# Kernel tuning notes

Measured on AMD Instinct MI355X. Metric: run time of the kernel, lower is better.

## Reference

```python
import jax, jax.numpy as jnp
import numpy as np

HIDDEN = 96


def setup_inputs() -> dict:
    key = jax.random.key(0)
    ks = jax.random.split(key, 7)
    B, T, H = 32, 16384, HIDDEN
    s = 1.0 / np.sqrt(H)  # torch LSTM init scale
    return {
        "x": jax.random.normal(ks[0], (B, T, 1), dtype=jnp.float32),
        "w_ih": jax.random.uniform(ks[1], (4 * H, 1), jnp.float32, -s, s),
        "w_hh": jax.random.uniform(ks[2], (4 * H, H), jnp.float32, -s, s),
        "b_ih": jax.random.uniform(ks[3], (4 * H,), jnp.float32, -s, s),
        "b_hh": jax.random.uniform(ks[4], (4 * H,), jnp.float32, -s, s),
        "w_dense": jax.random.uniform(ks[5], (1, H), jnp.float32, -s, s),
        "b_dense": jax.random.uniform(ks[6], (1,), jnp.float32, -s, s),
    }


def reference(x, w_ih, w_hh, b_ih, b_hh, w_dense, b_dense):
    # x: [B, T, 1]; single-layer LSTM (PyTorch gate order i, f, g, o),
    # zero initial hidden/cell state, then Linear(H -> 1) head.
    B, T, _ = x.shape
    H = w_hh.shape[1]
    b = b_ih + b_hh  # [4H]
    # Precompute input projection for all timesteps (input_size = 1).
    x_proj = jnp.einsum('btd,gd->btg', x, w_ih) + b  # [B, T, 4H]

    def step(carry, xp_t):
        h, c = carry
        gates = xp_t + h @ w_hh.T  # [B, 4H]
        i, f, g, o = jnp.split(gates, 4, axis=-1)
        i = jax.nn.sigmoid(i)
        f = jax.nn.sigmoid(f)
        g = jnp.tanh(g)
        o = jax.nn.sigmoid(o)
        c = f * c + i * g
        h = o * jnp.tanh(c)
        return (h, c), h

    h0 = jnp.zeros((B, H), dtype=x.dtype)
    c0 = jnp.zeros((B, H), dtype=x.dtype)
    _, hs = jax.lax.scan(step, (h0, c0), jnp.swapaxes(x_proj, 0, 1))  # hs: [T, B, H]
    hs = jnp.swapaxes(hs, 0, 1)  # [B, T, H]
    out = hs @ w_dense.T + b_dense  # [B, T, 1]; normalize_out=False -> no tanh
    return out
```

## Files before the change

### kernel.cpp

```cpp
#include <hip/hip_runtime.h>

typedef _Float16 h2 __attribute__((ext_vector_type(2)));

__device__ __forceinline__ h2 mkh2(float a, float b) {
    h2 r; r.x = (_Float16)a; r.y = (_Float16)b; return r;
}
__device__ __forceinline__ h2 bc(unsigned u) {
    union { unsigned u; h2 h; } c; c.u = u; return c.h;
}

template <int CTRL>
__device__ __forceinline__ float dpp_q(float v) {
    int i = __builtin_bit_cast(int, v);
    int r = __builtin_amdgcn_update_dpp(0, i, CTRL, 0xF, 0xF, true);
    return __builtin_bit_cast(float, r);
}

#define BARRIER() asm volatile("s_waitcnt lgkmcnt(0)\n\ts_barrier" ::: "memory")

#define DOT8(Q, i) do {                                               \
    aA0 = __builtin_amdgcn_fdot2(WA[4*i+0], bc(Q.x), aA0, false);     \
    aA1 = __builtin_amdgcn_fdot2(WA[4*i+1], bc(Q.y), aA1, false);     \
    aA2 = __builtin_amdgcn_fdot2(WA[4*i+2], bc(Q.z), aA2, false);     \
    aA3 = __builtin_amdgcn_fdot2(WA[4*i+3], bc(Q.w), aA3, false);     \
    aB0 = __builtin_amdgcn_fdot2(WB[4*i+0], bc(Q.x), aB0, false);     \
    aB1 = __builtin_amdgcn_fdot2(WB[4*i+1], bc(Q.y), aB1, false);     \
    aB2 = __builtin_amdgcn_fdot2(WB[4*i+2], bc(Q.z), aB2, false);     \
    aB3 = __builtin_amdgcn_fdot2(WB[4*i+3], bc(Q.w), aB3, false);     \
} while (0)

__device__ __forceinline__ float head_dot(const float* hrow, const float* wdp) {
    const float4* hr = reinterpret_cast<const float4*>(hrow);
    const float4* wv = reinterpret_cast<const float4*>(wdp);
    float a0 = 0.f, a1 = 0.f, a2 = 0.f, a3 = 0.f;
    #pragma unroll
    for (int k = 0; k < 24; k += 4) {
        float4 ha = hr[k], hb = hr[k + 1], hc = hr[k + 2], hd = hr[k + 3];
        float4 wa = wv[k], wb = wv[k + 1], wc = wv[k + 2], wd = wv[k + 3];
        a0 = fmaf(ha.w, wa.w, fmaf(ha.z, wa.z, fmaf(ha.y, wa.y, fmaf(ha.x, wa.x, a0))));
        a1 = fmaf(hb.w, wb.w, fmaf(hb.z, wb.z, fmaf(hb.y, wb.y, fmaf(hb.x, wb.x, a1))));
        a2 = fmaf(hc.w, wc.w, fmaf(hc.z, wc.z, fmaf(hc.y, wc.y, fmaf(hc.x, wc.x, a2))));
        a3 = fmaf(hd.w, wd.w, fmaf(hd.z, wd.z, fmaf(hd.y, wd.y, fmaf(hd.x, wd.x, a3))));
    }
    return (a0 + a1) + (a2 + a3);
}

__global__ __launch_bounds__(256)
void lstm_fused(
    const float* __restrict__ x,
    const float* __restrict__ w_ih,
    const float* __restrict__ w_hh,
    const float* __restrict__ b_ih,
    const float* __restrict__ b_hh,
    const float* __restrict__ w_dense,
    const float* __restrict__ b_dense,
    float* __restrict__ out,
    int T)
{
    const int tid  = threadIdx.x;
    const int lane = tid & 63;
    const int wv   = tid >> 6;

    __shared__ __align__(16) _Float16 hbuf[2][96];
    __shared__ __align__(16) float hist[2][64][100];

    if (tid < 96) { hbuf[0][tid] = (_Float16)0.f; hbuf[1][tid] = (_Float16)0.f; }

    const float* xrow = x + (size_t)blockIdx.x * T;
    float*       orow = out + (size_t)blockIdx.x * T;

    __syncthreads();

    if (wv < 3) {
        const int p = lane & 1;
        const int u = (wv << 5) | (lane >> 1);
        const int rowA = 96 * p + u;
        const int rowB = 96 * (2 + p) + u;

        h2 WA[48], WB[48];
        {
            const float4* ra = reinterpret_cast<const float4*>(w_hh + (size_t)rowA * 96);
            const float4* rb = reinterpret_cast<const float4*>(w_hh + (size_t)rowB * 96);
            #pragma unroll
            for (int q = 0; q < 24; ++q) {
                float4 fa = ra[q];
                WA[2*q]   = mkh2(fa.x, fa.y);
                WA[2*q+1] = mkh2(fa.z, fa.w);
            }
            #pragma unroll
            for (int q = 0; q < 24; ++q) {
                float4 fb = rb[q];
                WB[2*q]   = mkh2(fb.x, fb.y);
                WB[2*q+1] = mkh2(fb.z, fb.w);
            }
        }

        const float wihA  = w_ih[rowA];
        const float wihB  = w_ih[rowB];
        const float biasA = b_ih[rowA] + b_hh[rowA];
        const float biasB = b_ih[rowB] + b_hh[rowB];
        const float nkB = (p == 0) ? -2.885390082f : -1.442695041f;
        const float m1B = (p == 0) ? 2.f : 1.f;
        const float d1B = (p == 0) ? -1.f : 0.f;

        float c  = 0.f;
        float xs = xrow[0];

        #pragma unroll 1
        for (int t = 0; t < T; ++t) {
            int tn = (t + 1 < T) ? t + 1 : T - 1;
            float xs_n = xrow[tn];

            const uint4* hp = reinterpret_cast<const uint4*>(hbuf[(t & 1) ^ 1]);
            float aA0 = 0.f, aA1 = 0.f, aA2 = 0.f, aA3 = 0.f;
            float aB0 = 0.f, aB1 = 0.f, aB2 = 0.f, aB3 = 0.f;
            uint4 qA = hp[0], qB = hp[1], qC = hp[2];
            DOT8(qA, 0);  qA = hp[3];
            DOT8(qB, 1);  qB = hp[4];
            DOT8(qC, 2);  qC = hp[5];
            DOT8(qA, 3);  qA = hp[6];
            DOT8(qB, 4);  qB = hp[7];
            DOT8(qC, 5);  qC = hp[8];
            DOT8(qA, 6);  qA = hp[9];
            DOT8(qB, 7);  qB = hp[10];
            DOT8(qC, 8);  qC = hp[11];
            DOT8(qA, 9);
            DOT8(qB, 10);
            DOT8(qC, 11);

            float vA = (aA0 + aA1) + (aA2 + aA3);
            float vB = (aB0 + aB1) + (aB2 + aB3);
            float preA = vA + fmaf(xs, wihA, biasA);
            float preB = vB + fmaf(xs, wihB, biasB);
            float actA = __builtin_amdgcn_rcpf(1.f + __builtin_exp2f(preA * -1.442695041f));
            float actB = fmaf(m1B, __builtin_amdgcn_rcpf(1.f + __builtin_exp2f(preB * nkB)), d1B);

            float oA = dpp_q<0xB1>(actA);
            float oB = dpp_q<0xB1>(actB);

            if (p == 0) {
                c = fmaf(oA, c, actA * actB);
                float th = fmaf(2.f, __builtin_amdgcn_rcpf(1.f + __builtin_exp2f(c * -2.885390082f)), -1.f);
                float h  = oB * th;
                hbuf[t & 1][u] = (_Float16)h;
                hist[(t >> 6) & 1][t & 63][u] = h;
            }
            BARRIER();
            xs = xs_n;
        }
    } else {
        const float bd = b_dense[0];
        #pragma unroll 1
        for (int t = 0; t < T; ++t) {
            if (t && (t & 63) == 0) {
                const int buf = ((t >> 6) - 1) & 1;
                float a = head_dot(&hist[buf][lane][0], w_dense);
                orow[t - 64 + lane] = a + bd;
            }
            BARRIER();
        }
        const int T0 = ((T - 1) >> 6) << 6;
        if (lane < T - T0) {
            const int buf = (T0 >> 6) & 1;
            float a = head_dot(&hist[buf][lane][0], w_dense);
            orow[T0 + lane] = a + bd;
        }
    }
}

extern "C" void kernel_launch(void* const* d_in, const int* in_sizes, int n_in,
                              void* d_out, int out_size, void* d_ws, size_t ws_size,
                              hipStream_t stream) {
    const float* x   = (const float*)d_in[0];
    const float* wih = (const float*)d_in[1];
    const float* whh = (const float*)d_in[2];
    const float* bih = (const float*)d_in[3];
    const float* bhh = (const float*)d_in[4];
    const float* wd  = (const float*)d_in[5];
    const float* bd  = (const float*)d_in[6];
    float* out = (float*)d_out;

    const int B = 32;
    const int T = in_sizes[0] / B;

    lstm_fused<<<dim3(B), dim3(256), 0, stream>>>(x, wih, whh, bih, bhh, wd, bd, out, T);
}
```

Measured before the change: 7.999 ms.

## Compute recurrent matvec with MFMA 16x16x32 f16 across six gate waves

Moves the per-step h·W_hh product from per-lane fdot2 chains onto MFMA instructions. The work is spread over six compute waves of 16 hidden units each, with the activation scale constants folded into the weights and bias. Gate values are picked out of the MFMA accumulator lanes and exchanged between lanes with DPP. The block grows to 448 threads, which adds waves to every per-step barrier. The MFMA approach wastes most of the matrix width, because only one batch column per block is useful.

```diff
diff --git a/kernel.cpp b/kernel.cpp
--- a/kernel.cpp
+++ b/kernel.cpp
@@ -1,13 +1,7 @@
 #include <hip/hip_runtime.h>
 
-typedef _Float16 h2 __attribute__((ext_vector_type(2)));
-
-__device__ __forceinline__ h2 mkh2(float a, float b) {
-    h2 r; r.x = (_Float16)a; r.y = (_Float16)b; return r;
-}
-__device__ __forceinline__ h2 bc(unsigned u) {
-    union { unsigned u; h2 h; } c; c.u = u; return c.h;
-}
+typedef _Float16 f16x8 __attribute__((ext_vector_type(8)));
+typedef float    f32x4 __attribute__((ext_vector_type(4)));
 
 template <int CTRL>
 __device__ __forceinline__ float dpp_q(float v) {
@@ -17,17 +11,6 @@
 }
 
 #define BARRIER() asm volatile("s_waitcnt lgkmcnt(0)\n\ts_barrier" ::: "memory")
-
-#define DOT8(Q, i) do {                                               \
-    aA0 = __builtin_amdgcn_fdot2(WA[4*i+0], bc(Q.x), aA0, false);     \
-    aA1 = __builtin_amdgcn_fdot2(WA[4*i+1], bc(Q.y), aA1, false);     \
-    aA2 = __builtin_amdgcn_fdot2(WA[4*i+2], bc(Q.z), aA2, false);     \
-    aA3 = __builtin_amdgcn_fdot2(WA[4*i+3], bc(Q.w), aA3, false);     \
-    aB0 = __builtin_amdgcn_fdot2(WB[4*i+0], bc(Q.x), aB0, false);     \
-    aB1 = __builtin_amdgcn_fdot2(WB[4*i+1], bc(Q.y), aB1, false);     \
-    aB2 = __builtin_amdgcn_fdot2(WB[4*i+2], bc(Q.z), aB2, false);     \
-    aB3 = __builtin_amdgcn_fdot2(WB[4*i+3], bc(Q.w), aB3, false);     \
-} while (0)
 
 __device__ __forceinline__ float head_dot(const float* hrow, const float* wdp) {
     const float4* hr = reinterpret_cast<const float4*>(hrow);
@@ -45,7 +28,7 @@
     return (a0 + a1) + (a2 + a3);
 }
 
-__global__ __launch_bounds__(256)
+__global__ __launch_bounds__(448)
 void lstm_fused(
     const float* __restrict__ x,
     const float* __restrict__ w_ih,
@@ -71,37 +54,41 @@
 
     __syncthreads();
 
-    if (wv < 3) {
-        const int p = lane & 1;
-        const int u = (wv << 5) | (lane >> 1);
-        const int rowA = 96 * p + u;
-        const int rowB = 96 * (2 + p) + u;
+    if (wv < 6) {
+        const int g    = lane & 3;
+        const int uq   = lane >> 2;
+        const int u    = wv * 16 + uq;
+        const int arow = lane & 15;
+        const int kg   = lane >> 4;
 
-        h2 WA[48], WB[48];
-        {
-            const float4* ra = reinterpret_cast<const float4*>(w_hh + (size_t)rowA * 96);
-            const float4* rb = reinterpret_cast<const float4*>(w_hh + (size_t)rowB * 96);
+        f16x8 A_[4][3];
+        #pragma unroll
+        for (int ct = 0; ct < 4; ++ct) {
+            const float nk = (ct == 2) ? -2.885390082f : -1.442695041f;
+            const float* rp = w_hh + (size_t)(96 * ct + 16 * wv + arow) * 96 + kg * 8;
             #pragma unroll
-            for (int q = 0; q < 24; ++q) {
-                float4 fa = ra[q];
-                WA[2*q]   = mkh2(fa.x, fa.y);
-                WA[2*q+1] = mkh2(fa.z, fa.w);
-            }
+            for (int kt = 0; kt < 3; ++kt)
+                #pragma unroll
+                for (int i = 0; i < 8; ++i)
+                    A_[ct][kt][i] = (_Float16)(nk * rp[kt * 32 + i]);
+        }
+
+        float wihs[4][4], biass[4][4];
+        #pragma unroll
+        for (int ct = 0; ct < 4; ++ct) {
+            const float nk = (ct == 2) ? -2.885390082f : -1.442695041f;
             #pragma unroll
-            for (int q = 0; q < 24; ++q) {
-                float4 fb = rb[q];
-                WB[2*q]   = mkh2(fb.x, fb.y);
-                WB[2*q+1] = mkh2(fb.z, fb.w);
+            for (int q = 0; q < 4; ++q) {
+                int j = 96 * ct + 16 * wv + kg * 4 + q;
+                wihs[ct][q]  = nk * w_ih[j];
+                biass[ct][q] = nk * (b_ih[j] + b_hh[j]);
             }
         }
 
-        const float wihA  = w_ih[rowA];
-        const float wihB  = w_ih[rowB];
-        const float biasA = b_ih[rowA] + b_hh[rowA];
-        const float biasB = b_ih[rowB] + b_hh[rowB];
-        const float nkB = (p == 0) ? -2.885390082f : -1.442695041f;
-        const float m1B = (p == 0) ? 2.f : 1.f;
-        const float d1B = (p == 0) ? -1.f : 0.f;
+        const float m1 = (g == 2) ? 2.f : 1.f;
+        const float d1 = (g == 2) ? -1.f : 0.f;
+        const bool  g1 = (g & 1) != 0, g2 = (g & 2) != 0;
+        const bool  u1 = (uq & 1) != 0, u2 = (uq & 2) != 0;
 
         float c  = 0.f;
         float xs = xrow[0];
@@ -111,37 +98,49 @@
             int tn = (t + 1 < T) ? t + 1 : T - 1;
             float xs_n = xrow[tn];
 
-            const uint4* hp = reinterpret_cast<const uint4*>(hbuf[(t & 1) ^ 1]);
-            float aA0 = 0.f, aA1 = 0.f, aA2 = 0.f, aA3 = 0.f;
-            float aB0 = 0.f, aB1 = 0.f, aB2 = 0.f, aB3 = 0.f;
-            uint4 qA = hp[0], qB = hp[1], qC = hp[2];
-            DOT8(qA, 0);  qA = hp[3];
-            DOT8(qB, 1);  qB = hp[4];
-            DOT8(qC, 2);  qC = hp[5];
-            DOT8(qA, 3);  qA = hp[6];
-            DOT8(qB, 4);  qB = hp[7];
-            DOT8(qC, 5);  qC = hp[8];
-            DOT8(qA, 6);  qA = hp[9];
-            DOT8(qB, 7);  qB = hp[10];
-            DOT8(qC, 8);  qC = hp[11];
-            DOT8(qA, 9);
-            DOT8(qB, 10);
-            DOT8(qC, 11);
+            f32x4 D0, D1, D2, D3;
+            #pragma unroll
+            for (int q = 0; q < 4; ++q) {
+                D0[q] = fmaf(xs, wihs[0][q], biass[0][q]);
+                D1[q] = fmaf(xs, wihs[1][q], biass[1][q]);
+                D2[q] = fmaf(xs, wihs[2][q], biass[2][q]);
+                D3[q] = fmaf(xs, wihs[3][q], biass[3][q]);
+            }
 
-            float vA = (aA0 + aA1) + (aA2 + aA3);
-            float vB = (aB0 + aB1) + (aB2 + aB3);
-            float preA = vA + fmaf(xs, wihA, biasA);
-            float preB = vB + fmaf(xs, wihB, biasB);
-            float actA = __builtin_amdgcn_rcpf(1.f + __builtin_exp2f(preA * -1.442695041f));
-            float actB = fmaf(m1B, __builtin_amdgcn_rcpf(1.f + __builtin_exp2f(preB * nkB)), d1B);
+            const _Float16* hb = hbuf[(t & 1) ^ 1];
+            f16x8 B0 = *(const f16x8*)&hb[ 0 + kg * 8];
+            f16x8 B1 = *(const f16x8*)&hb[32 + kg * 8];
+            f16x8 B2 = *(const f16x8*)&hb[64 + kg * 8];
 
-            float oA = dpp_q<0xB1>(actA);
-            float oB = dpp_q<0xB1>(actB);
+            D0 = __builtin_amdgcn_mfma_f32_16x16x32_f16(A_[0][0], B0, D0, 0, 0, 0);
+            D1 = __builtin_amdgcn_mfma_f32_16x16x32_f16(A_[1][0], B0, D1, 0, 0, 0);
+            D2 = __builtin_amdgcn_mfma_f32_16x16x32_f16(A_[2][0], B0, D2, 0, 0, 0);
+            D3 = __builtin_amdgcn_mfma_f32_16x16x32_f16(A_[3][0], B0, D3, 0, 0, 0);
+            D0 = __builtin_amdgcn_mfma_f32_16x16x32_f16(A_[0][1], B1, D0, 0, 0, 0);
+            D1 = __builtin_amdgcn_mfma_f32_16x16x32_f16(A_[1][1], B1, D1, 0, 0, 0);
+            D2 = __builtin_amdgcn_mfma_f32_16x16x32_f16(A_[2][1], B1, D2, 0, 0, 0);
+            D3 = __builtin_amdgcn_mfma_f32_16x16x32_f16(A_[3][1], B1, D3, 0, 0, 0);
+            D0 = __builtin_amdgcn_mfma_f32_16x16x32_f16(A_[0][2], B2, D0, 0, 0, 0);
+            D1 = __builtin_amdgcn_mfma_f32_16x16x32_f16(A_[1][2], B2, D1, 0, 0, 0);
+            D2 = __builtin_amdgcn_mfma_f32_16x16x32_f16(A_[2][2], B2, D2, 0, 0, 0);
+            D3 = __builtin_amdgcn_mfma_f32_16x16x32_f16(A_[3][2], B2, D3, 0, 0, 0);
 
-            if (p == 0) {
-                c = fmaf(oA, c, actA * actB);
+            float s0 = g1 ? (g2 ? D3[0] : D1[0]) : (g2 ? D2[0] : D0[0]);
+            float s1 = g1 ? (g2 ? D3[1] : D1[1]) : (g2 ? D2[1] : D0[1]);
+            float s2 = g1 ? (g2 ? D3[2] : D1[2]) : (g2 ? D2[2] : D0[2]);
+            float s3 = g1 ? (g2 ? D3[3] : D1[3]) : (g2 ? D2[3] : D0[3]);
+            float pre = u1 ? (u2 ? s3 : s1) : (u2 ? s2 : s0);
+
+            float actv = fmaf(m1, __builtin_amdgcn_rcpf(1.f + __builtin_exp2f(pre)), d1);
+
+            float x1 = dpp_q<0xB1>(actv);
+            float x2 = dpp_q<0x4E>(actv);
+            float x3 = dpp_q<0x1B>(actv);
+
+            if (g == 0) {
+                c = fmaf(x1, c, actv * x2);
                 float th = fmaf(2.f, __builtin_amdgcn_rcpf(1.f + __builtin_exp2f(c * -2.885390082f)), -1.f);
-                float h  = oB * th;
+                float h  = x3 * th;
                 hbuf[t & 1][u] = (_Float16)h;
                 hist[(t >> 6) & 1][t & 63][u] = h;
             }
@@ -183,5 +182,5 @@
     const int B = 32;
     const int T = in_sizes[0] / B;
 
-    lstm_fused<<<dim3(B), dim3(256), 0, stream>>>(x, wih, whh, bih, bhh, wd, bd, out, T);
+    lstm_fused<<<dim3(B), dim3(448), 0, stream>>>(x, wih, whh, bih, bhh, wd, bd, out, T);
 }
```

Measured after the change: 8.378 ms. +4.7%, slower.

## Replace per-step block barrier with LDS flag spin-wait synchronization

Applied to the files above, without the earlier changes.

Swaps the per-timestep s_barrier across all four waves for sequence counters in shared memory. Each recurrent wave publishes its step and spins until the other two have caught up, and the head wave waits only at 64-step window boundaries. The goal is to take the head wave out of every step's barrier and let waves run with looser coupling. The cost is extra LDS polling traffic each step, and the spin loops have iteration caps that could silently break correctness if they time out. Visibility of the LDS writes relies only on lgkmcnt waits and volatile accesses.

```diff
diff --git a/kernel.cpp b/kernel.cpp
--- a/kernel.cpp
+++ b/kernel.cpp
@@ -15,8 +15,6 @@
     int r = __builtin_amdgcn_update_dpp(0, i, CTRL, 0xF, 0xF, true);
     return __builtin_bit_cast(float, r);
 }
-
-#define BARRIER() asm volatile("s_waitcnt lgkmcnt(0)\n\ts_barrier" ::: "memory")
 
 #define DOT8(Q, i) do {                                               \
     aA0 = __builtin_amdgcn_fdot2(WA[4*i+0], bc(Q.x), aA0, false);     \
@@ -28,6 +26,8 @@
     aB2 = __builtin_amdgcn_fdot2(WB[4*i+2], bc(Q.z), aB2, false);     \
     aB3 = __builtin_amdgcn_fdot2(WB[4*i+3], bc(Q.w), aB3, false);     \
 } while (0)
+
+#define LGKM0() asm volatile("s_waitcnt lgkmcnt(0)" ::: "memory")
 
 __device__ __forceinline__ float head_dot(const float* hrow, const float* wdp) {
     const float4* hr = reinterpret_cast<const float4*>(hrow);
@@ -63,13 +63,17 @@
 
     __shared__ __align__(16) _Float16 hbuf[2][96];
     __shared__ __align__(16) float hist[2][64][100];
+    __shared__ __align__(16) unsigned seqf[4];
 
     if (tid < 96) { hbuf[0][tid] = (_Float16)0.f; hbuf[1][tid] = (_Float16)0.f; }
+    if (tid < 4)  seqf[tid] = 0u;
 
     const float* xrow = x + (size_t)blockIdx.x * T;
     float*       orow = out + (size_t)blockIdx.x * T;
 
     __syncthreads();
+
+    volatile unsigned* sf = seqf;
 
     if (wv < 3) {
         const int p = lane & 1;
@@ -108,6 +112,24 @@
 
         #pragma unroll 1
         for (int t = 0; t < T; ++t) {
+            {
+                const unsigned need = (unsigned)t;
+                #pragma unroll 1
+                for (int spin = 0; spin < (1 << 18); ++spin) {
+                    if (sf[0] >= need && sf[1] >= need && sf[2] >= need) break;
+                }
+            }
+            if ((t & 63) == 0) {
+                const int w = t >> 6;
+                if (w >= 2) {
+                    const unsigned need = (unsigned)(w - 1);
+                    #pragma unroll 1
+                    for (int spin = 0; spin < (1 << 18); ++spin) {
+                        if (sf[3] >= need) break;
+                    }
+                }
+            }
+
             int tn = (t + 1 < T) ? t + 1 : T - 1;
             float xs_n = xrow[tn];
 
@@ -145,25 +167,37 @@
                 hbuf[t & 1][u] = (_Float16)h;
                 hist[(t >> 6) & 1][t & 63][u] = h;
             }
-            BARRIER();
+
+            LGKM0();
+            if (lane == 0) sf[wv] = (unsigned)(t + 1);
             xs = xs_n;
         }
     } else {
         const float bd = b_dense[0];
+        const int nwin = T >> 6;
         #pragma unroll 1
-        for (int t = 0; t < T; ++t) {
-            if (t && (t & 63) == 0) {
-                const int buf = ((t >> 6) - 1) & 1;
-                float a = head_dot(&hist[buf][lane][0], w_dense);
-                orow[t - 64 + lane] = a + bd;
-            }
-            BARRIER();
-        }
-        const int T0 = ((T - 1) >> 6) << 6;
-        if (lane < T - T0) {
-            const int buf = (T0 >> 6) & 1;
-            float a = head_dot(&hist[buf][lane][0], w_dense);
-            orow[T0 + lane] = a + bd;
+        for (int w = 0; w < nwin; ++w) {
+            const unsigned need = (unsigned)((w + 1) << 6);
+            #pragma unroll 1
+            for (int spin = 0; spin < (1 << 20); ++spin) {
+                if (sf[0] >= need && sf[1] >= need && sf[2] >= need) break;
+            }
+            float a = head_dot(&hist[w & 1][lane][0], w_dense);
+            orow[(w << 6) + lane] = a + bd;
+            LGKM0();
+            if (lane == 0) sf[3] = (unsigned)(w + 1);
+        }
+        const int T0 = nwin << 6;
+        if (T0 < T) {
+            const unsigned need = (unsigned)T;
+            #pragma unroll 1
+            for (int spin = 0; spin < (1 << 20); ++spin) {
+                if (sf[0] >= need && sf[1] >= need && sf[2] >= need) break;
+            }
+            if (lane < T - T0) {
+                float a = head_dot(&hist[nwin & 1][lane][0], w_dense);
+                orow[T0 + lane] = a + bd;
+            }
         }
     }
 }
```

Result: slower. 11.95 ms (+49.4%).

## Prefetch own-wave hidden-state chunks before the barrier to shorten the post-barrier LDS reads

Applied to the files above, without the earlier changes.

Each recurrent wave now issues LDS loads for the four h chunks it just wrote before hitting the per-step barrier. The barrier waits only until at most four LDS ops are outstanding, so those loads are in flight across it. After the barrier, only the other waves' eight chunks still need to be read. The W_hh register layout is rotated per wave so these prefetched chunks line up with the first dot products. The head wave keeps a full-drain barrier, and launch bounds now declare one block per CU. Correctness relies on in-order LDS counter semantics, so the earlier stores complete before the wave reaches the barrier.

```diff
diff --git a/kernel.cpp b/kernel.cpp
--- a/kernel.cpp
+++ b/kernel.cpp
@@ -16,8 +16,6 @@
     return __builtin_bit_cast(float, r);
 }
 
-#define BARRIER() asm volatile("s_waitcnt lgkmcnt(0)\n\ts_barrier" ::: "memory")
-
 #define DOT8(Q, i) do {                                               \
     aA0 = __builtin_amdgcn_fdot2(WA[4*i+0], bc(Q.x), aA0, false);     \
     aA1 = __builtin_amdgcn_fdot2(WA[4*i+1], bc(Q.y), aA1, false);     \
@@ -28,6 +26,9 @@
     aB2 = __builtin_amdgcn_fdot2(WB[4*i+2], bc(Q.z), aB2, false);     \
     aB3 = __builtin_amdgcn_fdot2(WB[4*i+3], bc(Q.w), aB3, false);     \
 } while (0)
+
+#define BARRIER4() asm volatile("s_waitcnt lgkmcnt(4)\n\ts_barrier" ::: "memory")
+#define BARRIER0() asm volatile("s_waitcnt lgkmcnt(0)\n\ts_barrier" ::: "memory")
 
 __device__ __forceinline__ float head_dot(const float* hrow, const float* wdp) {
     const float4* hr = reinterpret_cast<const float4*>(hrow);
@@ -45,7 +46,7 @@
     return (a0 + a1) + (a2 + a3);
 }
 
-__global__ __launch_bounds__(256)
+__global__ __launch_bounds__(256, 1)
 void lstm_fused(
     const float* __restrict__ x,
     const float* __restrict__ w_ih,
@@ -82,16 +83,14 @@
             const float4* ra = reinterpret_cast<const float4*>(w_hh + (size_t)rowA * 96);
             const float4* rb = reinterpret_cast<const float4*>(w_hh + (size_t)rowB * 96);
             #pragma unroll
-            for (int q = 0; q < 24; ++q) {
-                float4 fa = ra[q];
-                WA[2*q]   = mkh2(fa.x, fa.y);
-                WA[2*q+1] = mkh2(fa.z, fa.w);
-            }
-            #pragma unroll
-            for (int q = 0; q < 24; ++q) {
-                float4 fb = rb[q];
-                WB[2*q]   = mkh2(fb.x, fb.y);
-                WB[2*q+1] = mkh2(fb.z, fb.w);
+            for (int j = 0; j < 12; ++j) {
+                int cc = 4 * wv + j; if (cc >= 12) cc -= 12;
+                float4 fa = ra[2 * cc], ga = ra[2 * cc + 1];
+                WA[4*j+0] = mkh2(fa.x, fa.y); WA[4*j+1] = mkh2(fa.z, fa.w);
+                WA[4*j+2] = mkh2(ga.x, ga.y); WA[4*j+3] = mkh2(ga.z, ga.w);
+                float4 fb = rb[2 * cc], gb = rb[2 * cc + 1];
+                WB[4*j+0] = mkh2(fb.x, fb.y); WB[4*j+1] = mkh2(fb.z, fb.w);
+                WB[4*j+2] = mkh2(gb.x, gb.y); WB[4*j+3] = mkh2(gb.z, gb.w);
             }
         }
 
@@ -103,8 +102,21 @@
         const float m1B = (p == 0) ? 2.f : 1.f;
         const float d1B = (p == 0) ? -1.f : 0.f;
 
+        int c4  = 4*wv + 4;  if (c4  >= 12) c4  -= 12;
+        int c5  = 4*wv + 5;  if (c5  >= 12) c5  -= 12;
+        int c6  = 4*wv + 6;  if (c6  >= 12) c6  -= 12;
+        int c7  = 4*wv + 7;  if (c7  >= 12) c7  -= 12;
+        int c8  = 4*wv + 8;  if (c8  >= 12) c8  -= 12;
+        int c9  = 4*wv + 9;  if (c9  >= 12) c9  -= 12;
+        int c10 = 4*wv + 10; if (c10 >= 12) c10 -= 12;
+        int c11 = 4*wv + 11; if (c11 >= 12) c11 -= 12;
+
         float c  = 0.f;
         float xs = xrow[0];
+
+        const uint4* hp0 = reinterpret_cast<const uint4*>(hbuf[1]);
+        uint4 qO0 = hp0[4*wv + 0], qO1 = hp0[4*wv + 1];
+        uint4 qO2 = hp0[4*wv + 2], qO3 = hp0[4*wv + 3];
 
         #pragma unroll 1
         for (int t = 0; t < T; ++t) {
@@ -112,21 +124,14 @@
             float xs_n = xrow[tn];
 
             const uint4* hp = reinterpret_cast<const uint4*>(hbuf[(t & 1) ^ 1]);
+            uint4 qA = hp[c4],  qB = hp[c5],  qC = hp[c6],  qD = hp[c7];
+            uint4 qE = hp[c8],  qF = hp[c9],  qG = hp[c10], qH = hp[c11];
+
             float aA0 = 0.f, aA1 = 0.f, aA2 = 0.f, aA3 = 0.f;
             float aB0 = 0.f, aB1 = 0.f, aB2 = 0.f, aB3 = 0.f;
-            uint4 qA = hp[0], qB = hp[1], qC = hp[2];
-            DOT8(qA, 0);  qA = hp[3];
-            DOT8(qB, 1);  qB = hp[4];
-            DOT8(qC, 2);  qC = hp[5];
-            DOT8(qA, 3);  qA = hp[6];
-            DOT8(qB, 4);  qB = hp[7];
-            DOT8(qC, 5);  qC = hp[8];
-            DOT8(qA, 6);  qA = hp[9];
-            DOT8(qB, 7);  qB = hp[10];
-            DOT8(qC, 8);  qC = hp[11];
-            DOT8(qA, 9);
-            DOT8(qB, 10);
-            DOT8(qC, 11);
+            DOT8(qO0, 0); DOT8(qO1, 1); DOT8(qO2, 2); DOT8(qO3, 3);
+            DOT8(qA, 4);  DOT8(qB, 5);  DOT8(qC, 6);  DOT8(qD, 7);
+            DOT8(qE, 8);  DOT8(qF, 9);  DOT8(qG, 10); DOT8(qH, 11);
 
             float vA = (aA0 + aA1) + (aA2 + aA3);
             float vB = (aB0 + aB1) + (aB2 + aB3);
@@ -145,7 +150,13 @@
                 hbuf[t & 1][u] = (_Float16)h;
                 hist[(t >> 6) & 1][t & 63][u] = h;
             }
-            BARRIER();
+
+            __builtin_amdgcn_sched_barrier(0);
+            const uint4* hw = reinterpret_cast<const uint4*>(hbuf[t & 1]);
+            qO0 = hw[4*wv + 0]; qO1 = hw[4*wv + 1];
+            qO2 = hw[4*wv + 2]; qO3 = hw[4*wv + 3];
+
+            BARRIER4();
             xs = xs_n;
         }
     } else {
@@ -157,7 +168,7 @@
                 float a = head_dot(&hist[buf][lane][0], w_dense);
                 orow[t - 64 + lane] = a + bd;
             }
-            BARRIER();
+            BARRIER0();
         }
         const int T0 = ((T - 1) >> 6) << 6;
         if (lane < T - T0) {
```

Result: faster. 7.793 ms (-2.6%).
